# Optimization experiments

Hardware: AMD Instinct MI355X
Metric: run time of the kernel (lower is better)

## Reference

```python
import jax, jax.numpy as jnp
import numpy as np

B, I, H = 4096, 1024, 2048
EPS = 1e-5  # nn.GroupNorm default eps


def setup_inputs() -> dict:
    key = jax.random.key(0)
    ks = jax.random.split(key, 16)
    s_in = 1.0 / np.sqrt(I)
    s_h = 1.0 / np.sqrt(H)
    inp = {
        "x": jax.random.normal(ks[0], (B, I), jnp.float32),
        "h_prev": jax.random.normal(ks[1], (B, H), jnp.float32),
        "c_prev": jax.random.normal(ks[2], (B, H), jnp.float32),
        "n_prev": jnp.ones((B, H), jnp.float32),
        "m_prev": jax.random.normal(ks[3], (B, H), jnp.float32),
        # W_* : Linear(I, H) weight [H, I] + bias [H]
        "Wi": jax.random.uniform(ks[4], (H, I), jnp.float32, -s_in, s_in),
        "Wf": jax.random.uniform(ks[5], (H, I), jnp.float32, -s_in, s_in),
        "Wz": jax.random.uniform(ks[6], (H, I), jnp.float32, -s_in, s_in),
        "Wo": jax.random.uniform(ks[7], (H, I), jnp.float32, -s_in, s_in),
        "bi": jax.random.uniform(ks[8], (H,), jnp.float32, -s_in, s_in),
        "bf": jax.random.uniform(ks[9], (H,), jnp.float32, -s_in, s_in),
        "bz": jax.random.uniform(ks[10], (H,), jnp.float32, -s_in, s_in),
        "bo": jax.random.uniform(ks[11], (H,), jnp.float32, -s_in, s_in),
        # R_* : Linear(H, H, bias=False) weight [H, H]
        "Ri": jax.random.uniform(ks[12], (H, H), jnp.float32, -s_h, s_h),
        "Rf": jax.random.uniform(ks[13], (H, H), jnp.float32, -s_h, s_h),
        "Rz": jax.random.uniform(ks[14], (H, H), jnp.float32, -s_h, s_h),
        "Ro": jax.random.uniform(ks[15], (H, H), jnp.float32, -s_h, s_h),
        # GroupNorm(1, H) affine params
        "gn_w": jnp.ones((H,), jnp.float32),
        "gn_b": jnp.zeros((H,), jnp.float32),
    }
    return inp


def _group_norm1(x, w, b):
    # GroupNorm with 1 group on [B, H]: normalize over all H per sample
    mu = jnp.mean(x, axis=-1, keepdims=True)
    var = jnp.mean(jnp.square(x - mu), axis=-1, keepdims=True)
    return (x - mu) * jax.lax.rsqrt(var + EPS) * w + b


def reference(x, h_prev, c_prev, n_prev, m_prev,
              Wi, Wf, Wz, Wo, bi, bf, bz, bo,
              Ri, Rf, Rz, Ro, gn_w, gn_b):
    # Batch the 4 input and 4 recurrent GEMMs into one each: [B, 4H]
    Wcat = jnp.concatenate([Wi, Wf, Wz, Wo], axis=0)   # [4H, I]
    bcat = jnp.concatenate([bi, bf, bz, bo], axis=0)   # [4H]
    Rcat = jnp.concatenate([Ri, Rf, Rz, Ro], axis=0)   # [4H, H]
    pre = x @ Wcat.T + bcat + h_prev @ Rcat.T          # [B, 4H]
    pi, pf, pz, po = jnp.split(pre, 4, axis=-1)
    i = jax.nn.sigmoid(pi)
    f = jax.nn.sigmoid(pf)
    z = jnp.tanh(pz)
    o = jax.nn.sigmoid(po)
    m = jnp.maximum(f * m_prev, i)
    c = f * c_prev + i * z
    n = f * n_prev + i
    c_stab = c / n
    h = o * jnp.tanh(_group_norm1(c_stab, gn_w, gn_b))
    return (h, c, n, m)
```

## Files before the change

kernel.cpp:

```cpp
#include <hip/hip_runtime.h>
#include <hip/hip_bf16.h>
#include <math.h>

#define B_ 4096
#define I_ 1024
#define H_ 2048
#define K_ 3072
#define N4 8192
#define EPSGN 1e-5f

#define NT_K 48
#define PANB 16384
#define LDSB 65536

typedef __bf16 bf16;
typedef __bf16 bf16x8 __attribute__((ext_vector_type(8)));
typedef float  f32x4  __attribute__((ext_vector_type(4)));

__device__ __forceinline__ float sigm(float x) {
  return 1.0f / (1.0f + __expf(-x));
}
__device__ __forceinline__ float tanh_fast(float x) {
  float a = fabsf(x);
  float e = __expf(-2.0f * a);
  float t = (1.0f - e) / (1.0f + e);
  return copysignf(t, x);
}

__global__ void convA(const float* __restrict__ x, const float* __restrict__ hp,
                      char* __restrict__ At) {
  int sid = blockIdx.x * blockDim.x + threadIdx.x;
  int p = sid & 1023;
  int pan = sid >> 10;
  int mt = pan / 96;
  int rem = pan - mt * 96;
  int kt = rem >> 1;
  int h = rem & 1;
  int r = p >> 3;
  int ks = (p & 7) ^ (r & 7);
  int row = mt * 256 + h * 128 + r;
  int k = kt * 64 + ks * 8;
  const float* src = (k < I_) ? (x + (size_t)row * I_ + k)
                              : (hp + (size_t)row * H_ + (k - I_));
  f32x4 v0 = *(const f32x4*)src;
  f32x4 v1 = *(const f32x4*)(src + 4);
  bf16x8 o;
  o[0]=(bf16)v0[0]; o[1]=(bf16)v0[1]; o[2]=(bf16)v0[2]; o[3]=(bf16)v0[3];
  o[4]=(bf16)v1[0]; o[5]=(bf16)v1[1]; o[6]=(bf16)v1[2]; o[7]=(bf16)v1[3];
  *(bf16x8*)(At + (size_t)sid * 16) = o;
}

__global__ void convB(const float* __restrict__ Wi, const float* __restrict__ Wf,
                      const float* __restrict__ Wz, const float* __restrict__ Wo,
                      const float* __restrict__ Ri, const float* __restrict__ Rf,
                      const float* __restrict__ Rz, const float* __restrict__ Ro,
                      char* __restrict__ Bt) {
  int sid = blockIdx.x * blockDim.x + threadIdx.x;
  int p = sid & 1023;
  int pan = sid >> 10;
  int nt = pan / 96;
  int rem = pan - nt * 96;
  int kt = rem >> 1;
  int h = rem & 1;
  int r = p >> 3;
  int ks = (p & 7) ^ (r & 7);
  int n = nt * 256 + h * 128 + r;
  int g = n >> 11;
  int hr = n & 2047;
  int k = kt * 64 + ks * 8;
  const float* Wp = (g == 0) ? Wi : (g == 1) ? Wf : (g == 2) ? Wz : Wo;
  const float* Rp = (g == 0) ? Ri : (g == 1) ? Rf : (g == 2) ? Rz : Ro;
  const float* src = (k < I_) ? (Wp + (size_t)hr * I_ + k)
                              : (Rp + (size_t)hr * H_ + (k - I_));
  f32x4 v0 = *(const f32x4*)src;
  f32x4 v1 = *(const f32x4*)(src + 4);
  bf16x8 o;
  o[0]=(bf16)v0[0]; o[1]=(bf16)v0[1]; o[2]=(bf16)v0[2]; o[3]=(bf16)v0[3];
  o[4]=(bf16)v1[0]; o[5]=(bf16)v1[1]; o[6]=(bf16)v1[2]; o[7]=(bf16)v1[3];
  *(bf16x8*)(Bt + (size_t)sid * 16) = o;
}

__device__ __forceinline__ void gload16(const char* g, char* l) {
  __builtin_amdgcn_global_load_lds(
      (const __attribute__((address_space(1))) void*)g,
      (__attribute__((address_space(3))) void*)l, 16, 0, 0);
}
__device__ __forceinline__ void stage(const char* g, char* l) {
  gload16(g, l);
  gload16(g + 8192, l + 8192);
}

__global__ __launch_bounds__(512, 2) void gemm8(const char* __restrict__ At,
                                                const char* __restrict__ Bt,
                                                float* __restrict__ pre) {
  extern __shared__ char lds[];
  const int tid = threadIdx.x;
  const int lane = tid & 63;
  const int wv = tid >> 6;
  const int wm = wv >> 2;
  const int wn = wv & 3;

  int bid = (blockIdx.x & 7) * 64 + (blockIdx.x >> 3);
  const int bm = bid >> 5;
  const int bn = bid & 31;

  const char* a_src = At + (size_t)bm * (NT_K * 2 * PANB) + tid * 16;
  const char* b_src = Bt + (size_t)bn * (NT_K * 2 * PANB) + tid * 16;
  char* a_lds = lds + tid * 16;
  char* b_lds = lds + LDSB + tid * 16;

  const int l15 = lane & 15;
  const int l7  = lane & 7;
  const int q   = lane >> 4;
  int offk[2];
  offk[0] = l15 * 128 + (((0 + q) ^ l7) << 4);
  offk[1] = l15 * 128 + (((4 + q) ^ l7) << 4);

  const char* apan_base = lds + wm * PANB;
  const char* bpan_base = lds + LDSB + (wn >> 1) * PANB;
  const int bcol = (wn & 1) * 8192;

  f32x4 acc[8][4] = {};
  bf16x8 af[4][2], bfr[2][2][2];

  stage(b_src + 0 * PANB, b_lds + 0 * PANB);
  stage(b_src + 1 * PANB, b_lds + 1 * PANB);
  stage(a_src + 0 * PANB, a_lds + 0 * PANB);
  stage(a_src + 1 * PANB, a_lds + 1 * PANB);
  stage(b_src + 2 * PANB, b_lds + 2 * PANB);
  stage(b_src + 3 * PANB, b_lds + 3 * PANB);
  asm volatile("s_waitcnt vmcnt(4)" ::: "memory");
  __builtin_amdgcn_s_barrier();

#pragma unroll 2
  for (int t = 0; t < NT_K; ++t) {
    const int par = (t & 1) * 2;
    const char* apan = apan_base + par * PANB;
    const char* bpan = bpan_base + par * PANB;

#pragma unroll
    for (int fi = 0; fi < 4; ++fi)
#pragma unroll
      for (int ks = 0; ks < 2; ++ks)
        af[fi][ks] = *(const bf16x8*)(apan + fi * 2048 + offk[ks]);
#pragma unroll
    for (int fj = 0; fj < 2; ++fj)
#pragma unroll
      for (int ks = 0; ks < 2; ++ks)
        bfr[0][fj][ks] = *(const bf16x8*)(bpan + bcol + fj * 2048 + offk[ks]);
    if (t + 1 < NT_K)
      stage(a_src + (size_t)(t + 1) * 2 * PANB,
            a_lds + (((t + 1) & 1) * 2) * PANB);
    __builtin_amdgcn_s_barrier();
    asm volatile("s_waitcnt lgkmcnt(0)" ::: "memory");
    __builtin_amdgcn_s_setprio(1);
#pragma unroll
    for (int fi = 0; fi < 4; ++fi)
#pragma unroll
      for (int fj = 0; fj < 2; ++fj)
#pragma unroll
        for (int ks = 0; ks < 2; ++ks)
          acc[fi][fj] = __builtin_amdgcn_mfma_f32_16x16x32_bf16(
              af[fi][ks], bfr[0][fj][ks], acc[fi][fj], 0, 0, 0);
    __builtin_amdgcn_s_setprio(0);
    __builtin_amdgcn_s_barrier();

#pragma unroll
    for (int fj = 0; fj < 2; ++fj)
#pragma unroll
      for (int ks = 0; ks < 2; ++ks)
        bfr[1][fj][ks] = *(const bf16x8*)(bpan + bcol + 4096 + fj * 2048 + offk[ks]);
    if (t + 1 < NT_K)
      stage(a_src + (size_t)(t + 1) * 2 * PANB + PANB,
            a_lds + ((((t + 1) & 1) * 2) + 1) * PANB);
    __builtin_amdgcn_s_barrier();
    asm volatile("s_waitcnt lgkmcnt(0)" ::: "memory");
    __builtin_amdgcn_s_setprio(1);
#pragma unroll
    for (int fi = 0; fi < 4; ++fi)
#pragma unroll
      for (int fj = 0; fj < 2; ++fj)
#pragma unroll
        for (int ks = 0; ks < 2; ++ks)
          acc[fi][2 + fj] = __builtin_amdgcn_mfma_f32_16x16x32_bf16(
              af[fi][ks], bfr[1][fj][ks], acc[fi][2 + fj], 0, 0, 0);
    __builtin_amdgcn_s_setprio(0);
    __builtin_amdgcn_s_barrier();

#pragma unroll
    for (int fi = 0; fi < 4; ++fi)
#pragma unroll
      for (int ks = 0; ks < 2; ++ks)
        af[fi][ks] = *(const bf16x8*)(apan + 8192 + fi * 2048 + offk[ks]);
    if (t + 2 < NT_K)
      stage(b_src + (size_t)(t + 2) * 2 * PANB,
            b_lds + par * PANB);
    __builtin_amdgcn_s_barrier();
    asm volatile("s_waitcnt lgkmcnt(0)" ::: "memory");
    __builtin_amdgcn_s_setprio(1);
#pragma unroll
    for (int fi = 0; fi < 4; ++fi)
#pragma unroll
      for (int fj = 0; fj < 2; ++fj)
#pragma unroll
        for (int ks = 0; ks < 2; ++ks)
          acc[4 + fi][2 + fj] = __builtin_amdgcn_mfma_f32_16x16x32_bf16(
              af[fi][ks], bfr[1][fj][ks], acc[4 + fi][2 + fj], 0, 0, 0);
    __builtin_amdgcn_s_setprio(0);
    __builtin_amdgcn_s_barrier();

    if (t + 2 < NT_K)
      stage(b_src + (size_t)(t + 2) * 2 * PANB + PANB,
            b_lds + (par + 1) * PANB);
    __builtin_amdgcn_s_barrier();
    asm volatile("s_waitcnt lgkmcnt(0)" ::: "memory");
    __builtin_amdgcn_s_setprio(1);
#pragma unroll
    for (int fi = 0; fi < 4; ++fi)
#pragma unroll
      for (int fj = 0; fj < 2; ++fj)
#pragma unroll
        for (int ks = 0; ks < 2; ++ks)
          acc[4 + fi][fj] = __builtin_amdgcn_mfma_f32_16x16x32_bf16(
              af[fi][ks], bfr[0][fj][ks], acc[4 + fi][fj], 0, 0, 0);
    __builtin_amdgcn_s_setprio(0);
    if (t < NT_K - 2)
      asm volatile("s_waitcnt vmcnt(4)" ::: "memory");
    else
      asm volatile("s_waitcnt vmcnt(0)" ::: "memory");
    __builtin_amdgcn_s_barrier();
  }

  const int crow0 = (lane >> 4) * 4;
  const int ccol  = lane & 15;
#pragma unroll
  for (int mi = 0; mi < 8; ++mi)
#pragma unroll
    for (int nj = 0; nj < 4; ++nj)
#pragma unroll
      for (int j = 0; j < 4; ++j) {
        int row = bm * 256 + wm * 128 + mi * 16 + crow0 + j;
        int col = bn * 256 + wn * 64 + nj * 16 + ccol;
        pre[(size_t)row * N4 + col] = acc[mi][nj][j];
      }
}

__global__ void eltwise(const float* __restrict__ pre,
                        const float* __restrict__ bi, const float* __restrict__ bfp,
                        const float* __restrict__ bz, const float* __restrict__ bo,
                        const float* __restrict__ c_prev, const float* __restrict__ n_prev,
                        const float* __restrict__ m_prev,
                        float* __restrict__ out) {
  long e = ((long)blockIdx.x * blockDim.x + threadIdx.x) * 4;
  if (e >= (long)B_ * H_) return;
  int b = (int)(e / H_);
  int h = (int)(e % H_);
  const long PL = (long)B_ * H_;

  f32x4 PI = *(const f32x4*)(pre + (long)b * N4 + 0 * H_ + h);
  f32x4 PF = *(const f32x4*)(pre + (long)b * N4 + 1 * H_ + h);
  f32x4 PZ = *(const f32x4*)(pre + (long)b * N4 + 2 * H_ + h);
  f32x4 BI = *(const f32x4*)(bi + h);
  f32x4 BF = *(const f32x4*)(bfp + h);
  f32x4 BZ = *(const f32x4*)(bz + h);
  f32x4 CP = *(const f32x4*)(c_prev + e);
  f32x4 NP = *(const f32x4*)(n_prev + e);
  f32x4 MP = *(const f32x4*)(m_prev + e);

  f32x4 C, N, M;
#pragma unroll
  for (int j = 0; j < 4; ++j) {
    float ig = sigm(PI[j] + BI[j]);
    float fg = sigm(PF[j] + BF[j]);
    float zg = tanh_fast(PZ[j] + BZ[j]);
    M[j] = fmaxf(fg * MP[j], ig);
    C[j] = fg * CP[j] + ig * zg;
    N[j] = fg * NP[j] + ig;
  }
  *(f32x4*)(out + PL * 1 + e) = C;
  *(f32x4*)(out + PL * 2 + e) = N;
  *(f32x4*)(out + PL * 3 + e) = M;
  (void)bo;
}

__global__ __launch_bounds__(256) void gnorm(const float* __restrict__ pre,
                                             const float* __restrict__ bo,
                                             const float* __restrict__ gnw,
                                             const float* __restrict__ gnb,
                                             float* __restrict__ out) {
  const int b = blockIdx.x;
  const int t = threadIdx.x;
  const long PL = (long)B_ * H_;
  const float* crow = out + PL * 1 + (long)b * H_;
  const float* nrow = out + PL * 2 + (long)b * H_;

  float cs[8];
  float sum = 0.f, sq = 0.f;
#pragma unroll
  for (int j = 0; j < 8; ++j) {
    int hh = t + j * 256;
    float v = crow[hh] / nrow[hh];
    cs[j] = v;
    sum += v;
    sq  += v * v;
  }
#pragma unroll
  for (int off = 1; off < 64; off <<= 1) {
    sum += __shfl_xor(sum, off);
    sq  += __shfl_xor(sq, off);
  }
  __shared__ float s1[4], s2[4];
  const int wv = t >> 6, lane = t & 63;
  if (lane == 0) { s1[wv] = sum; s2[wv] = sq; }
  __syncthreads();
  sum = s1[0] + s1[1] + s1[2] + s1[3];
  sq  = s2[0] + s2[1] + s2[2] + s2[3];
  const float mu  = sum * (1.0f / H_);
  const float var = sq * (1.0f / H_) - mu * mu;
  const float rinv = rsqrtf(var + EPSGN);

#pragma unroll
  for (int j = 0; j < 8; ++j) {
    int hh = t + j * 256;
    float po = pre[(long)b * N4 + 3 * H_ + hh] + bo[hh];
    float o = sigm(po);
    float g = (cs[j] - mu) * rinv * gnw[hh] + gnb[hh];
    out[(long)b * H_ + hh] = o * tanh_fast(g);
  }
}

extern "C" void kernel_launch(void* const* d_in, const int* in_sizes, int n_in,
                              void* d_out, int out_size, void* d_ws, size_t ws_size,
                              hipStream_t stream) {
  const float* x      = (const float*)d_in[0];
  const float* h_prev = (const float*)d_in[1];
  const float* c_prev = (const float*)d_in[2];
  const float* n_prev = (const float*)d_in[3];
  const float* m_prev = (const float*)d_in[4];
  const float* Wi = (const float*)d_in[5];
  const float* Wf = (const float*)d_in[6];
  const float* Wz = (const float*)d_in[7];
  const float* Wo = (const float*)d_in[8];
  const float* bi = (const float*)d_in[9];
  const float* bf = (const float*)d_in[10];
  const float* bz = (const float*)d_in[11];
  const float* bo = (const float*)d_in[12];
  const float* Ri = (const float*)d_in[13];
  const float* Rf = (const float*)d_in[14];
  const float* Rz = (const float*)d_in[15];
  const float* Ro = (const float*)d_in[16];
  const float* gnw = (const float*)d_in[17];
  const float* gnb = (const float*)d_in[18];

  char* ws = (char*)d_ws;
  char* At = ws;
  char* Bt = ws + (size_t)B_ * K_ * 2;
  float* pre = (float*)(ws + (size_t)B_ * K_ * 2 + (size_t)N4 * K_ * 2);
  float* out = (float*)d_out;

  static bool attr_set = false;
  (void)attr_set;
  hipFuncSetAttribute((const void*)gemm8,
                      hipFuncAttributeMaxDynamicSharedMemorySize, 131072);

  convA<<<((size_t)B_ * K_ / 8) / 256, 256, 0, stream>>>(x, h_prev, At);
  convB<<<((size_t)N4 * K_ / 8) / 256, 256, 0, stream>>>(Wi, Wf, Wz, Wo,
                                                         Ri, Rf, Rz, Ro, Bt);
  gemm8<<<512, 512, 131072, stream>>>(At, Bt, pre);
  eltwise<<<(B_ * H_ / 4) / 256, 256, 0, stream>>>(pre, bi, bf, bz, bo,
                                                   c_prev, n_prev, m_prev, out);
  gnorm<<<B_, 256, 0, stream>>>(pre, bo, gnw, gnb, out);
}
```

Before: 308.5 us.

## Store GEMM preactivations as bf16 and fuse gate eltwise with group norm

The GEMM now writes the preactivation matrix in bf16 instead of fp32, halving that intermediate's write and read traffic. The separate eltwise and group-norm kernels are merged into one per-row kernel. It computes the gates, c, n and m, reduces the statistics of c/n and writes h without re-reading c and n from memory. The cost is extra rounding error on the preactivations before bias and nonlinearity.

```diff
diff --git a/kernel.cpp b/kernel.cpp
--- a/kernel.cpp
+++ b/kernel.cpp
@@ -92,7 +92,7 @@
 
 __global__ __launch_bounds__(512, 2) void gemm8(const char* __restrict__ At,
                                                 const char* __restrict__ Bt,
-                                                float* __restrict__ pre) {
+                                                bf16* __restrict__ pre) {
   extern __shared__ char lds[];
   const int tid = threadIdx.x;
   const int lane = tid & 63;
@@ -241,69 +241,67 @@
       for (int j = 0; j < 4; ++j) {
         int row = bm * 256 + wm * 128 + mi * 16 + crow0 + j;
         int col = bn * 256 + wn * 64 + nj * 16 + ccol;
-        pre[(size_t)row * N4 + col] = acc[mi][nj][j];
+        pre[(size_t)row * N4 + col] = (bf16)acc[mi][nj][j];
       }
 }
 
-__global__ void eltwise(const float* __restrict__ pre,
-                        const float* __restrict__ bi, const float* __restrict__ bfp,
-                        const float* __restrict__ bz, const float* __restrict__ bo,
-                        const float* __restrict__ c_prev, const float* __restrict__ n_prev,
-                        const float* __restrict__ m_prev,
-                        float* __restrict__ out) {
-  long e = ((long)blockIdx.x * blockDim.x + threadIdx.x) * 4;
-  if (e >= (long)B_ * H_) return;
-  int b = (int)(e / H_);
-  int h = (int)(e % H_);
-  const long PL = (long)B_ * H_;
-
-  f32x4 PI = *(const f32x4*)(pre + (long)b * N4 + 0 * H_ + h);
-  f32x4 PF = *(const f32x4*)(pre + (long)b * N4 + 1 * H_ + h);
-  f32x4 PZ = *(const f32x4*)(pre + (long)b * N4 + 2 * H_ + h);
-  f32x4 BI = *(const f32x4*)(bi + h);
-  f32x4 BF = *(const f32x4*)(bfp + h);
-  f32x4 BZ = *(const f32x4*)(bz + h);
-  f32x4 CP = *(const f32x4*)(c_prev + e);
-  f32x4 NP = *(const f32x4*)(n_prev + e);
-  f32x4 MP = *(const f32x4*)(m_prev + e);
-
-  f32x4 C, N, M;
-#pragma unroll
-  for (int j = 0; j < 4; ++j) {
-    float ig = sigm(PI[j] + BI[j]);
-    float fg = sigm(PF[j] + BF[j]);
-    float zg = tanh_fast(PZ[j] + BZ[j]);
-    M[j] = fmaxf(fg * MP[j], ig);
-    C[j] = fg * CP[j] + ig * zg;
-    N[j] = fg * NP[j] + ig;
-  }
-  *(f32x4*)(out + PL * 1 + e) = C;
-  *(f32x4*)(out + PL * 2 + e) = N;
-  *(f32x4*)(out + PL * 3 + e) = M;
-  (void)bo;
-}
-
-__global__ __launch_bounds__(256) void gnorm(const float* __restrict__ pre,
-                                             const float* __restrict__ bo,
-                                             const float* __restrict__ gnw,
-                                             const float* __restrict__ gnb,
-                                             float* __restrict__ out) {
+__global__ __launch_bounds__(256) void fusedpost(
+    const bf16* __restrict__ pre,
+    const float* __restrict__ bi, const float* __restrict__ bfp,
+    const float* __restrict__ bz, const float* __restrict__ bo,
+    const float* __restrict__ c_prev, const float* __restrict__ n_prev,
+    const float* __restrict__ m_prev,
+    const float* __restrict__ gnw, const float* __restrict__ gnb,
+    float* __restrict__ out) {
   const int b = blockIdx.x;
   const int t = threadIdx.x;
+  const int h0 = t * 8;
   const long PL = (long)B_ * H_;
-  const float* crow = out + PL * 1 + (long)b * H_;
-  const float* nrow = out + PL * 2 + (long)b * H_;
-
-  float cs[8];
+  const long e = (long)b * H_ + h0;
+  const bf16* prow = pre + (size_t)b * N4;
+
+  bf16x8 PI = *(const bf16x8*)(prow + 0 * H_ + h0);
+  bf16x8 PF = *(const bf16x8*)(prow + 1 * H_ + h0);
+  bf16x8 PZ = *(const bf16x8*)(prow + 2 * H_ + h0);
+  bf16x8 PO = *(const bf16x8*)(prow + 3 * H_ + h0);
+  f32x4 BI0 = *(const f32x4*)(bi + h0),  BI1 = *(const f32x4*)(bi + h0 + 4);
+  f32x4 BF0 = *(const f32x4*)(bfp + h0), BF1 = *(const f32x4*)(bfp + h0 + 4);
+  f32x4 BZ0 = *(const f32x4*)(bz + h0),  BZ1 = *(const f32x4*)(bz + h0 + 4);
+  f32x4 BO0 = *(const f32x4*)(bo + h0),  BO1 = *(const f32x4*)(bo + h0 + 4);
+  f32x4 CP0 = *(const f32x4*)(c_prev + e), CP1 = *(const f32x4*)(c_prev + e + 4);
+  f32x4 NP0 = *(const f32x4*)(n_prev + e), NP1 = *(const f32x4*)(n_prev + e + 4);
+  f32x4 MP0 = *(const f32x4*)(m_prev + e), MP1 = *(const f32x4*)(m_prev + e + 4);
+
+  float cs[8], og[8];
+  f32x4 C0, C1, N0, N1, M0, M1;
   float sum = 0.f, sq = 0.f;
 #pragma unroll
   for (int j = 0; j < 8; ++j) {
-    int hh = t + j * 256;
-    float v = crow[hh] / nrow[hh];
+    float pi = (float)PI[j] + ((j < 4) ? BI0[j] : BI1[j - 4]);
+    float pf = (float)PF[j] + ((j < 4) ? BF0[j] : BF1[j - 4]);
+    float pz = (float)PZ[j] + ((j < 4) ? BZ0[j] : BZ1[j - 4]);
+    float po = (float)PO[j] + ((j < 4) ? BO0[j] : BO1[j - 4]);
+    float cp = (j < 4) ? CP0[j] : CP1[j - 4];
+    float np = (j < 4) ? NP0[j] : NP1[j - 4];
+    float mp = (j < 4) ? MP0[j] : MP1[j - 4];
+    float ig = sigm(pi);
+    float fg = sigm(pf);
+    float zg = tanh_fast(pz);
+    og[j] = sigm(po);
+    float m = fmaxf(fg * mp, ig);
+    float c = fg * cp + ig * zg;
+    float n = fg * np + ig;
+    if (j < 4) { C0[j] = c; N0[j] = n; M0[j] = m; }
+    else       { C1[j-4] = c; N1[j-4] = n; M1[j-4] = m; }
+    float v = c / n;
     cs[j] = v;
     sum += v;
     sq  += v * v;
   }
+  *(f32x4*)(out + PL * 1 + e) = C0; *(f32x4*)(out + PL * 1 + e + 4) = C1;
+  *(f32x4*)(out + PL * 2 + e) = N0; *(f32x4*)(out + PL * 2 + e + 4) = N1;
+  *(f32x4*)(out + PL * 3 + e) = M0; *(f32x4*)(out + PL * 3 + e + 4) = M1;
+
 #pragma unroll
   for (int off = 1; off < 64; off <<= 1) {
     sum += __shfl_xor(sum, off);
@@ -319,14 +317,19 @@
   const float var = sq * (1.0f / H_) - mu * mu;
   const float rinv = rsqrtf(var + EPSGN);
 
+  f32x4 GW0 = *(const f32x4*)(gnw + h0), GW1 = *(const f32x4*)(gnw + h0 + 4);
+  f32x4 GB0 = *(const f32x4*)(gnb + h0), GB1 = *(const f32x4*)(gnb + h0 + 4);
+  f32x4 Hh0, Hh1;
 #pragma unroll
   for (int j = 0; j < 8; ++j) {
-    int hh = t + j * 256;
-    float po = pre[(long)b * N4 + 3 * H_ + hh] + bo[hh];
-    float o = sigm(po);
-    float g = (cs[j] - mu) * rinv * gnw[hh] + gnb[hh];
-    out[(long)b * H_ + hh] = o * tanh_fast(g);
+    float gw = (j < 4) ? GW0[j] : GW1[j - 4];
+    float gb = (j < 4) ? GB0[j] : GB1[j - 4];
+    float g = (cs[j] - mu) * rinv * gw + gb;
+    float hv = og[j] * tanh_fast(g);
+    if (j < 4) Hh0[j] = hv; else Hh1[j - 4] = hv;
   }
+  *(f32x4*)(out + e) = Hh0;
+  *(f32x4*)(out + e + 4) = Hh1;
 }
 
 extern "C" void kernel_launch(void* const* d_in, const int* in_sizes, int n_in,
@@ -355,11 +358,9 @@
   char* ws = (char*)d_ws;
   char* At = ws;
   char* Bt = ws + (size_t)B_ * K_ * 2;
-  float* pre = (float*)(ws + (size_t)B_ * K_ * 2 + (size_t)N4 * K_ * 2);
+  bf16* pre = (bf16*)(ws + (size_t)B_ * K_ * 2 + (size_t)N4 * K_ * 2);
   float* out = (float*)d_out;
 
-  static bool attr_set = false;
-  (void)attr_set;
   hipFuncSetAttribute((const void*)gemm8,
                       hipFuncAttributeMaxDynamicSharedMemorySize, 131072);
 
@@ -367,7 +368,6 @@
   convB<<<((size_t)N4 * K_ / 8) / 256, 256, 0, stream>>>(Wi, Wf, Wz, Wo,
                                                          Ri, Rf, Rz, Ro, Bt);
   gemm8<<<512, 512, 131072, stream>>>(At, Bt, pre);
-  eltwise<<<(B_ * H_ / 4) / 256, 256, 0, stream>>>(pre, bi, bf, bz, bo,
-                                                   c_prev, n_prev, m_prev, out);
-  gnorm<<<B_, 256, 0, stream>>>(pre, bo, gnw, gnb, out);
-}
+  fusedpost<<<B_, 256, 0, stream>>>(pre, bi, bf, bz, bo,
+                                    c_prev, n_prev, m_prev, gnw, gnb, out);
+}
```

Result: faster. 290.1 us (-6.0%).
